# Kernel optimization log

Measured on AMD Instinct MI355X. Metric: run time of the kernel, lower is better.

The kernel has to match this reference:

```python
import jax, jax.numpy as jnp
import numpy as np

V, E, DIN, DH = 8192, 4096, 512, 256
N_CLASSES = 2
EPS = 1e-5  # torch LayerNorm default
EDGE_P = 0.004  # ~33 nodes per hyperedge


def layernorm(x, g, b):
    m = jnp.mean(x, axis=-1, keepdims=True)
    v = jnp.mean((x - m) ** 2, axis=-1, keepdims=True)
    return (x - m) / jnp.sqrt(v + EPS) * g + b


def setup_inputs() -> dict:
    key = jax.random.key(0)
    ks = jax.random.split(key, 8)
    X = jax.random.normal(ks[0], (V, DIN), dtype=jnp.float32)
    # binary incidence matrix (|V|, |E|)
    H_inc = (jax.random.uniform(ks[1], (V, E)) < EDGE_P).astype(jnp.float32)
    Wp = jax.random.normal(ks[2], (DH, DIN), dtype=jnp.float32) * 0.02  # input_proj (no bias)
    W0 = jax.random.normal(ks[3], (DH, DH), dtype=jnp.float32) * 0.02
    W1 = jax.random.normal(ks[4], (DH, DH), dtype=jnp.float32) * 0.02
    g0 = jnp.ones((DH,), jnp.float32); b0 = jnp.zeros((DH,), jnp.float32)
    g1 = jnp.ones((DH,), jnp.float32); b1 = jnp.zeros((DH,), jnp.float32)
    Wc = jax.random.normal(ks[5], (N_CLASSES, DH), dtype=jnp.float32) * 0.02
    bc = jnp.zeros((N_CLASSES,), jnp.float32)
    return {"X": X, "H_inc": H_inc, "Wp": Wp, "W0": W0, "W1": W1,
            "g0": g0, "b0": b0, "g1": g1, "b1": b1, "Wc": Wc, "bc": bc}


def reference(X, H_inc, Wp, W0, W1, g0, b0, g1, b1, Wc, bc):
    # --- normalized incidence: H_tilde = D_v^{-1/2} H D_e^{-1/2}, 0 for isolated ---
    d_v = H_inc.sum(axis=1)   # (V,)
    d_e = H_inc.sum(axis=0)   # (E,)
    dvi = jnp.where(d_v > 0, jnp.where(d_v > 0, d_v, 1.0) ** -0.5, 0.0)
    dei = jnp.where(d_e > 0, jnp.where(d_e > 0, d_e, 1.0) ** -0.5, 0.0)
    H_tilde = dvi[:, None] * H_inc * dei[None, :]            # (V, E)
    HHt = H_tilde @ H_tilde.T                                # (V, V)

    # input projection
    Xh = X @ Wp.T                                            # (V, DH)

    # L=2 message-passing layers with residual + LayerNorm
    for W, g, b in ((W0, g0, b0), (W1, g1, b1)):
        Xn = jax.nn.relu((HHt @ Xh) @ W.T)
        Xh = layernorm(Xh + Xn, g, b)

    # mean pool per hyperedge (== Python loop over E in the original):
    # z_e = mean of member node embeddings; zeros for empty hyperedges
    cnt = jnp.where(d_e > 0, d_e, 1.0)[:, None]              # (E, 1)
    z_E = (H_inc.T @ Xh) / cnt                               # (E, DH)

    logits = z_E @ Wc.T + bc                                 # (E, 2)
    return jax.nn.softmax(logits, axis=1)
```

## Files before the change

kernel.cpp:

```cpp
#include <hip/hip_runtime.h>
#include <math.h>

#define NV 8192
#define NE 4096
#define DIN 512
#define DH 256
#define CAP_E 96
#define CAP_V 64
#define NPROJ (NV / 32)
#define NSCAN (NV / 2)

#define OFF_XH   0
#define OFF_UB   (OFF_XH + NV*DH)
#define OFF_YB   (OFF_UB + NV*DH/2)
#define OFF_NCNT (OFF_YB + NE*DH/2)
#define OFF_ECNT (OFF_NCNT + NV)
#define OFF_EL   (OFF_ECNT + NE*16)
#define OFF_NL   (OFF_EL + NE*CAP_E)
#define OFF_XHB  (OFF_NL + NV*CAP_V)

using bf16x8 = __attribute__((ext_vector_type(8))) short;
using f32x4  = __attribute__((ext_vector_type(4))) float;
using f32x4v = __attribute__((ext_vector_type(4))) float;

__device__ inline unsigned short f2bf(float f) {
    union { float f; unsigned u; } v; v.f = f;
    unsigned r = v.u + 0x7FFF + ((v.u >> 16) & 1);
    return (unsigned short)(r >> 16);
}
__device__ inline float b2f(unsigned short s) {
    union { unsigned u; float f; } v; v.u = ((unsigned)s) << 16; return v.f;
}

__global__ __launch_bounds__(256) void scan_proj(const float* __restrict__ H,
                                                 const float* __restrict__ X,
                                                 const float* __restrict__ Wp,
                                                 float* __restrict__ Xh,
                                                 unsigned short* __restrict__ Xhb,
                                                 int* __restrict__ edge_cnt,
                                                 int* __restrict__ node_cnt,
                                                 int* __restrict__ edge_list,
                                                 int* __restrict__ node_list) {
    __shared__ short AsBs[1024 + 8192];
    const int tid = threadIdx.x;
    if (blockIdx.x >= NPROJ) {
        const int w = tid >> 6, lane = tid & 63;
        const int v    = (blockIdx.x - NPROJ) * 2 + (w >> 1);
        const int half = w & 1;
        const f32x4v* H4 = (const f32x4v*)(H + (size_t)v * NE) + half * 512;
        f32x4v h[8];
#pragma unroll
        for (int it = 0; it < 8; ++it)
            h[it] = __builtin_nontemporal_load(&H4[lane + 64 * it]);
        unsigned m = 0u;
#pragma unroll
        for (int it = 0; it < 8; ++it) {
#pragma unroll
            for (int c = 0; c < 4; ++c)
                m |= (h[it][c] != 0.0f ? 1u : 0u) << (it * 4 + c);
        }
        int n = __builtin_popcount(m);
        int pre = n;
#pragma unroll
        for (int o = 1; o < 64; o <<= 1) {
            int t = __shfl_up(pre, o, 64);
            if (lane >= o) pre += t;
        }
        int total = __shfl(pre, 63, 64);
        int local = pre - n;
        int base = 0;
        if (lane == 0 && total > 0) base = atomicAdd(&node_cnt[v], total);
        base = __shfl(base, 0, 64) + local;
        const int ebase = half * 2048 + 4 * lane;
        int e_arr[4] = {0, 0, 0, 0};
        {
            unsigned mm = m;
#pragma unroll
            for (int u = 0; u < 4; ++u) {
                if (mm) {
                    int j = __builtin_ctz(mm);
                    mm &= mm - 1;
                    e_arr[u] = ebase + 256 * (j >> 2) + (j & 3);
                }
            }
        }
        int s_arr[4];
#pragma unroll
        for (int u = 0; u < 4; ++u)
            s_arr[u] = (u < n) ? atomicAdd(&edge_cnt[e_arr[u] << 4], 1) : 0;
#pragma unroll
        for (int u = 0; u < 4; ++u) {
            if (u < n) {
                if (s_arr[u] < CAP_E) edge_list[e_arr[u] * CAP_E + s_arr[u]] = v;
                int idx = base + u;
                if (idx < CAP_V) node_list[v * CAP_V + idx] = e_arr[u];
            }
        }
        if (n > 4) {
            unsigned mm = m;
            mm &= mm - 1; mm &= mm - 1; mm &= mm - 1; mm &= mm - 1;
            int k = 4;
            while (mm) {
                int j = __builtin_ctz(mm); mm &= mm - 1;
                int ee = ebase + 256 * (j >> 2) + (j & 3);
                int gc = atomicAdd(&edge_cnt[ee << 4], 1);
                if (gc < CAP_E) edge_list[ee * CAP_E + gc] = v;
                int idx = base + k;
                if (idx < CAP_V) node_list[v * CAP_V + idx] = ee;
                ++k;
            }
        }
        return;
    }
    short* As = AsBs;
    short* Bs = AsBs + 1024;
    const int K = DIN;
    const int lane = tid & 63;
    const int w    = tid >> 6;
    const int bm   = blockIdx.x * 32;
    const int swz  = lane ^ ((lane >> 3) & 6);
    float4 ar, br[8];
    ar = *(const float4*)(X + (size_t)(bm + (tid >> 3)) * K + ((tid & 7) << 2));
#pragma unroll
    for (int it = 0; it < 8; ++it) {
        int i = tid + it * 256;
        br[it] = *(const float4*)(Wp + (size_t)(i >> 3) * K + ((i & 7) << 2));
    }
    f32x4 acc[2][4];
#pragma unroll
    for (int mi = 0; mi < 2; ++mi)
#pragma unroll
        for (int ni = 0; ni < 4; ++ni) acc[mi][ni] = (f32x4){0.f, 0.f, 0.f, 0.f};
    for (int k0 = 0; k0 < K; k0 += 32) {
        __syncthreads();
        {
            int row = tid >> 3, kk = (tid & 7) << 2;
            int quad = kk >> 3, j = kk & 7;
            int ln = (row & 15) + (quad << 4);
            int pp = ln ^ ((ln >> 3) & 6);
            ushort4 u = {f2bf(ar.x), f2bf(ar.y), f2bf(ar.z), f2bf(ar.w)};
            *(ushort4*)&As[(row >> 4) * 512 + pp * 8 + j] = u;
        }
#pragma unroll
        for (int it = 0; it < 8; ++it) {
            int i = tid + it * 256;
            int row = i >> 3, kk = (i & 7) << 2;
            int quad = kk >> 3, j = kk & 7;
            int ln = (row & 15) + (quad << 4);
            int pp = ln ^ ((ln >> 3) & 6);
            float4 v = br[it];
            ushort4 u = {f2bf(v.x), f2bf(v.y), f2bf(v.z), f2bf(v.w)};
            *(ushort4*)&Bs[(row >> 4) * 512 + pp * 8 + j] = u;
        }
        __syncthreads();
        if (k0 + 32 < K) {
            int kn = k0 + 32;
            ar = *(const float4*)(X + (size_t)(bm + (tid >> 3)) * K + kn + ((tid & 7) << 2));
#pragma unroll
            for (int it = 0; it < 8; ++it) {
                int i = tid + it * 256;
                br[it] = *(const float4*)(Wp + (size_t)(i >> 3) * K + kn + ((i & 7) << 2));
            }
        }
        bf16x8 af[2], bfr[4];
        af[0] = *(const bf16x8*)&As[0 * 512 + swz * 8];
        af[1] = *(const bf16x8*)&As[1 * 512 + swz * 8];
#pragma unroll
        for (int ni = 0; ni < 4; ++ni)
            bfr[ni] = *(const bf16x8*)&Bs[(w * 4 + ni) * 512 + swz * 8];
#pragma unroll
        for (int mi = 0; mi < 2; ++mi)
#pragma unroll
            for (int ni = 0; ni < 4; ++ni)
                acc[mi][ni] = __builtin_amdgcn_mfma_f32_16x16x32_bf16(
                    af[mi], bfr[ni], acc[mi][ni], 0, 0, 0);
    }
    const int quad = lane >> 4, cl = lane & 15;
#pragma unroll
    for (int mi = 0; mi < 2; ++mi)
#pragma unroll
        for (int ni = 0; ni < 4; ++ni)
#pragma unroll
            for (int r = 0; r < 4; ++r) {
                float v = acc[mi][ni][r];
                size_t idx = (size_t)(bm + mi * 16 + quad * 4 + r) * DH + w * 64 + ni * 16 + cl;
                Xh[idx] = v;
                Xhb[idx] = f2bf(v);
            }
}

__global__ __launch_bounds__(256) void gemm_u(const unsigned short* __restrict__ A,
                                              const float* __restrict__ W,
                                              unsigned short* __restrict__ U) {
    const int K = DH;
    __shared__ short As[2048];
    __shared__ short Bs[16384];
    const int tid  = threadIdx.x;
    const int lane = tid & 63;
    const int w    = tid >> 6;
    const int bm   = blockIdx.x * 32;
    const int swz  = lane ^ ((lane >> 3) & 6);

    uint4 ar; float4 br[16];
    ar = *(const uint4*)(A + (size_t)(bm + (tid >> 3)) * K + ((tid & 7) << 3));
#pragma unroll
    for (int it = 0; it < 16; ++it) {
        int i = tid + it * 256;
        br[it] = *(const float4*)(W + (size_t)(i >> 4) * K + ((i & 15) << 2));
    }
    f32x4 acc[2][4];
#pragma unroll
    for (int mi = 0; mi < 2; ++mi)
#pragma unroll
        for (int ni = 0; ni < 4; ++ni) acc[mi][ni] = (f32x4){0.f, 0.f, 0.f, 0.f};

    for (int k0 = 0; k0 < K; k0 += 64) {
        __syncthreads();
        {
            int row = tid >> 3, kq = tid & 7;
            int kc = kq >> 2, quad = kq & 3;
            int ln = (row & 15) + (quad << 4);
            int pp = ln ^ ((ln >> 3) & 6);
            *(uint4*)&As[((row >> 4) * 2 + kc) * 512 + pp * 8] = ar;
        }
#pragma unroll
        for (int it = 0; it < 16; ++it) {
            int i = tid + it * 256;
            int row = i >> 4, kk = (i & 15) << 2;
            int kc = kk >> 5, quad = (kk >> 3) & 3, j = kk & 7;
            int ln = (row & 15) + (quad << 4);
            int pp = ln ^ ((ln >> 3) & 6);
            float4 v = br[it];
            ushort4 u = {f2bf(v.x), f2bf(v.y), f2bf(v.z), f2bf(v.w)};
            *(ushort4*)&Bs[((row >> 4) * 2 + kc) * 512 + pp * 8 + j] = u;
        }
        __syncthreads();
        if (k0 + 64 < K) {
            int kn = k0 + 64;
            ar = *(const uint4*)(A + (size_t)(bm + (tid >> 3)) * K + kn + ((tid & 7) << 3));
#pragma unroll
            for (int it = 0; it < 16; ++it) {
                int i = tid + it * 256;
                br[it] = *(const float4*)(W + (size_t)(i >> 4) * K + kn + ((i & 15) << 2));
            }
        }
#pragma unroll
        for (int kc = 0; kc < 2; ++kc) {
            bf16x8 af[2], bfr[4];
            af[0] = *(const bf16x8*)&As[(0 * 2 + kc) * 512 + swz * 8];
            af[1] = *(const bf16x8*)&As[(1 * 2 + kc) * 512 + swz * 8];
#pragma unroll
            for (int ni = 0; ni < 4; ++ni)
                bfr[ni] = *(const bf16x8*)&Bs[((w * 4 + ni) * 2 + kc) * 512 + swz * 8];
#pragma unroll
            for (int mi = 0; mi < 2; ++mi)
#pragma unroll
                for (int ni = 0; ni < 4; ++ni)
                    acc[mi][ni] = __builtin_amdgcn_mfma_f32_16x16x32_bf16(
                        af[mi], bfr[ni], acc[mi][ni], 0, 0, 0);
        }
    }
    const int quad = lane >> 4, cl = lane & 15;
#pragma unroll
    for (int mi = 0; mi < 2; ++mi)
#pragma unroll
        for (int ni = 0; ni < 4; ++ni)
#pragma unroll
            for (int r = 0; r < 4; ++r)
                U[(size_t)(bm + mi * 16 + quad * 4 + r) * DH + w * 64 + ni * 16 + cl]
                    = f2bf(acc[mi][ni][r]);
}

__global__ __launch_bounds__(64) void edge_gather(const unsigned short* __restrict__ Ub,
                                                  const int* __restrict__ edge_cnt,
                                                  const int* __restrict__ edge_list,
                                                  const int* __restrict__ node_cnt,
                                                  unsigned short* __restrict__ Yb) {
    int e = blockIdx.x;
    int tid = threadIdx.x;
    __shared__ int   lv[CAP_E];
    __shared__ float lc[CAP_E];
    int tc = edge_cnt[e << 4];
    int cnt = min(tc, CAP_E);
    for (int j = tid; j < cnt; j += 64) {
        int v = edge_list[e * CAP_E + j];
        lv[j] = v * (DH / 4);
        lc[j] = rsqrtf((float)node_cnt[v]);
    }
    __syncthreads();
    const ushort4* X4 = (const ushort4*)Ub;
    float4 a[8];
#pragma unroll
    for (int u = 0; u < 8; ++u) a[u] = (float4){0.f, 0.f, 0.f, 0.f};
    int i = 0;
    for (; i + 8 <= cnt; i += 8) {
#pragma unroll
        for (int u = 0; u < 8; ++u) {
            ushort4 h = X4[lv[i + u] + tid]; float c = lc[i + u];
            a[u].x = fmaf(c, b2f(h.x), a[u].x); a[u].y = fmaf(c, b2f(h.y), a[u].y);
            a[u].z = fmaf(c, b2f(h.z), a[u].z); a[u].w = fmaf(c, b2f(h.w), a[u].w);
        }
    }
    for (; i < cnt; ++i) {
        ushort4 h = X4[lv[i] + tid]; float c = lc[i];
        a[0].x = fmaf(c, b2f(h.x), a[0].x); a[0].y = fmaf(c, b2f(h.y), a[0].y);
        a[0].z = fmaf(c, b2f(h.z), a[0].z); a[0].w = fmaf(c, b2f(h.w), a[0].w);
    }
#pragma unroll
    for (int u = 4; u > 0; u >>= 1)
#pragma unroll
        for (int q = 0; q < u; ++q) {
            a[q].x += a[q + u].x; a[q].y += a[q + u].y;
            a[q].z += a[q + u].z; a[q].w += a[q + u].w;
        }
    float de = tc > 0 ? rsqrtf((float)tc) : 0.f;
    ushort4 o = {f2bf(de * a[0].x), f2bf(de * a[0].y),
                 f2bf(de * a[0].z), f2bf(de * a[0].w)};
    ((ushort4*)Yb)[e * (DH / 4) + tid] = o;
}

__global__ __launch_bounds__(64) void node_ln(const unsigned short* __restrict__ Yb,
                                              const int* __restrict__ node_cnt,
                                              const int* __restrict__ node_list,
                                              const int* __restrict__ edge_cnt,
                                              float* __restrict__ Xh,
                                              unsigned short* __restrict__ Xhb,
                                              const float* __restrict__ g,
                                              const float* __restrict__ b) {
    int v = blockIdx.x;
    int tid = threadIdx.x;
    __shared__ int   le[CAP_V];
    __shared__ float lc[CAP_V];
    int tc = node_cnt[v];
    int cnt = min(tc, CAP_V);
    if (tid < cnt) {
        int e = node_list[v * CAP_V + tid];
        le[tid] = e * (DH / 4);
        lc[tid] = rsqrtf((float)edge_cnt[e << 4]);
    }
    __syncthreads();
    const ushort4* Y4 = (const ushort4*)Yb;
    float4 a[8];
#pragma unroll
    for (int u = 0; u < 8; ++u) a[u] = (float4){0.f, 0.f, 0.f, 0.f};
    int i = 0;
    for (; i + 8 <= cnt; i += 8) {
#pragma unroll
        for (int u = 0; u < 8; ++u) {
            ushort4 h = Y4[le[i + u] + tid]; float c = lc[i + u];
            a[u].x = fmaf(c, b2f(h.x), a[u].x); a[u].y = fmaf(c, b2f(h.y), a[u].y);
            a[u].z = fmaf(c, b2f(h.z), a[u].z); a[u].w = fmaf(c, b2f(h.w), a[u].w);
        }
    }
    for (; i < cnt; ++i) {
        ushort4 h = Y4[le[i] + tid]; float c = lc[i];
        a[0].x = fmaf(c, b2f(h.x), a[0].x); a[0].y = fmaf(c, b2f(h.y), a[0].y);
        a[0].z = fmaf(c, b2f(h.z), a[0].z); a[0].w = fmaf(c, b2f(h.w), a[0].w);
    }
#pragma unroll
    for (int u = 4; u > 0; u >>= 1)
#pragma unroll
        for (int q = 0; q < u; ++q) {
            a[q].x += a[q + u].x; a[q].y += a[q + u].y;
            a[q].z += a[q + u].z; a[q].w += a[q + u].w;
        }
    float dv = tc > 0 ? rsqrtf((float)tc) : 0.f;
    float4 xr = ((const float4*)Xh)[v * (DH / 4) + tid];
    float x0 = xr.x + fmaxf(dv * a[0].x, 0.f);
    float x1 = xr.y + fmaxf(dv * a[0].y, 0.f);
    float x2 = xr.z + fmaxf(dv * a[0].z, 0.f);
    float x3 = xr.w + fmaxf(dv * a[0].w, 0.f);
    float s = (x0 + x1) + (x2 + x3);
    float q = fmaf(x0, x0, fmaf(x1, x1, fmaf(x2, x2, x3 * x3)));
#pragma unroll
    for (int o = 1; o < 64; o <<= 1) {
        s += __shfl_xor(s, o, 64);
        q += __shfl_xor(q, o, 64);
    }
    float m = s * (1.0f / DH);
    float var = q * (1.0f / DH) - m * m;
    float rstd = rsqrtf(var + 1e-5f);
    float4 g4 = ((const float4*)g)[tid];
    float4 b4 = ((const float4*)b)[tid];
    float4 o;
    o.x = (x0 - m) * rstd * g4.x + b4.x;
    o.y = (x1 - m) * rstd * g4.y + b4.y;
    o.z = (x2 - m) * rstd * g4.z + b4.z;
    o.w = (x3 - m) * rstd * g4.w + b4.w;
    ((float4*)Xh)[v * (DH / 4) + tid] = o;
    ushort4 ob = {f2bf(o.x), f2bf(o.y), f2bf(o.z), f2bf(o.w)};
    ((ushort4*)Xhb)[v * (DH / 4) + tid] = ob;
}

__global__ __launch_bounds__(64) void pool_classify(const unsigned short* __restrict__ Xhb,
                                                    const int* __restrict__ edge_cnt,
                                                    const int* __restrict__ edge_list,
                                                    const float* __restrict__ Wc,
                                                    const float* __restrict__ bc,
                                                    float* __restrict__ out) {
    int e = blockIdx.x;
    int tid = threadIdx.x;
    __shared__ int lv[CAP_E];
    int tc = edge_cnt[e << 4];
    int cnt = min(tc, CAP_E);
    for (int j = tid; j < cnt; j += 64) lv[j] = edge_list[e * CAP_E + j] * (DH / 4);
    __syncthreads();
    const ushort4* X4 = (const ushort4*)Xhb;
    float4 a[8];
#pragma unroll
    for (int u = 0; u < 8; ++u) a[u] = (float4){0, 0, 0, 0};
    int i = 0;
    for (; i + 8 <= cnt; i += 8) {
#pragma unroll
        for (int u = 0; u < 8; ++u) {
            ushort4 h = X4[lv[i + u] + tid];
            a[u].x += b2f(h.x); a[u].y += b2f(h.y);
            a[u].z += b2f(h.z); a[u].w += b2f(h.w);
        }
    }
    for (; i < cnt; ++i) {
        ushort4 h = X4[lv[i] + tid];
        a[0].x += b2f(h.x); a[0].y += b2f(h.y);
        a[0].z += b2f(h.z); a[0].w += b2f(h.w);
    }
#pragma unroll
    for (int u = 4; u > 0; u >>= 1)
#pragma unroll
        for (int q = 0; q < u; ++q) {
            a[q].x += a[q + u].x; a[q].y += a[q + u].y;
            a[q].z += a[q + u].z; a[q].w += a[q + u].w;
        }
    float inv = tc > 0 ? 1.0f / (float)tc : 1.0f;
    float4 val = {a[0].x * inv, a[0].y * inv, a[0].z * inv, a[0].w * inv};
    const float4* W4 = (const float4*)Wc;
    float4 w0 = W4[tid], w1 = W4[64 + tid];
    float p0 = val.x * w0.x + val.y * w0.y + val.z * w0.z + val.w * w0.w;
    float p1 = val.x * w1.x + val.y * w1.y + val.z * w1.z + val.w * w1.w;
#pragma unroll
    for (int o = 32; o > 0; o >>= 1) {
        p0 += __shfl_down(p0, o, 64);
        p1 += __shfl_down(p1, o, 64);
    }
    if (tid == 0) {
        float l0 = p0 + bc[0], l1 = p1 + bc[1];
        float mx = fmaxf(l0, l1);
        float e0 = expf(l0 - mx), e1 = expf(l1 - mx);
        float s = 1.0f / (e0 + e1);
        out[e * 2 + 0] = e0 * s;
        out[e * 2 + 1] = e1 * s;
    }
}

extern "C" void kernel_launch(void* const* d_in, const int* in_sizes, int n_in,
                              void* d_out, int out_size, void* d_ws, size_t ws_size,
                              hipStream_t stream) {
    const float* X  = (const float*)d_in[0];
    const float* H  = (const float*)d_in[1];
    const float* Wp = (const float*)d_in[2];
    const float* W0 = (const float*)d_in[3];
    const float* W1 = (const float*)d_in[4];
    const float* g0 = (const float*)d_in[5];
    const float* b0 = (const float*)d_in[6];
    const float* g1 = (const float*)d_in[7];
    const float* b1 = (const float*)d_in[8];
    const float* Wc = (const float*)d_in[9];
    const float* bc = (const float*)d_in[10];
    float* out = (float*)d_out;

    float* ws = (float*)d_ws;
    float* Xh  = ws + OFF_XH;
    unsigned short* Ub  = (unsigned short*)(ws + OFF_UB);
    unsigned short* Yb  = (unsigned short*)(ws + OFF_YB);
    int* node_cnt  = (int*)(ws + OFF_NCNT);
    int* edge_cnt  = (int*)(ws + OFF_ECNT);
    int* edge_list = (int*)(ws + OFF_EL);
    int* node_list = (int*)(ws + OFF_NL);
    unsigned short* Xhb = (unsigned short*)(ws + OFF_XHB);

    hipMemsetAsync(node_cnt, 0, (size_t)(NV + NE * 16) * sizeof(int), stream);

    scan_proj<<<NPROJ + NSCAN, 256, 0, stream>>>(H, X, Wp, Xh, Xhb,
                                                 edge_cnt, node_cnt, edge_list, node_list);

    const float* Ws[2] = {W0, W1};
    const float* gs[2] = {g0, g1};
    const float* bs[2] = {b0, b1};
    for (int l = 0; l < 2; ++l) {
        gemm_u<<<NV / 32, 256, 0, stream>>>(Xhb, Ws[l], Ub);
        edge_gather<<<NE, 64, 0, stream>>>(Ub, edge_cnt, edge_list, node_cnt, Yb);
        node_ln<<<NV, 64, 0, stream>>>(Yb, node_cnt, node_list, edge_cnt,
                                       Xh, Xhb, gs[l], bs[l]);
    }

    pool_classify<<<NE, 64, 0, stream>>>(Xhb, edge_cnt, edge_list, Wc, bc, out);
}
```

Baseline: 291.2 us.

## Fuse layer GEMMs into projection and layer-0 LayerNorm epilogues via LDS

The standalone gemm_u kernel is removed. The bf16 tile of the input projection (and later of the layer-0 LayerNorm output) is written straight into swizzled LDS, and the 32x256 @ W^T GEMM is run in the same block, reading W from global and converting it to bf16 per wave. This drops two launches and the round trip of Xhb through global memory. In exchange, node_ln_u uses only 256 blocks, and each wave gathers 8 node rows one after another. That cuts parallelism for the latency-bound gather, and W is re-read per block without LDS staging.

```diff
diff --git a/kernel.cpp b/kernel.cpp
--- a/kernel.cpp
+++ b/kernel.cpp
@@ -32,11 +32,59 @@
     union { unsigned u; float f; } v; v.u = ((unsigned)s) << 16; return v.f;
 }
 
+__device__ inline void u_gemm_from_lds(const short* __restrict__ sm,
+                                       const float* __restrict__ W,
+                                       unsigned short* __restrict__ Ub,
+                                       int bm, int tid) {
+    const int w = tid >> 6, lane = tid & 63;
+    const int r15 = lane & 15, k8 = (lane >> 4) << 3;
+    const int swz = lane ^ ((lane >> 3) & 6);
+    f32x4 acc[2][4];
+#pragma unroll
+    for (int mi = 0; mi < 2; ++mi)
+#pragma unroll
+        for (int ni = 0; ni < 4; ++ni) acc[mi][ni] = (f32x4){0.f, 0.f, 0.f, 0.f};
+#pragma unroll
+    for (int kc = 0; kc < 8; ++kc) {
+        bf16x8 af[2], bfr[4];
+        af[0] = *(const bf16x8*)&sm[(0 * 8 + kc) * 512 + swz * 8];
+        af[1] = *(const bf16x8*)&sm[(1 * 8 + kc) * 512 + swz * 8];
+#pragma unroll
+        for (int ni = 0; ni < 4; ++ni) {
+            const float* wr = W + (size_t)(w * 64 + ni * 16 + r15) * DH + kc * 32 + k8;
+            float4 b0 = *(const float4*)wr;
+            float4 b1 = *(const float4*)(wr + 4);
+            bf16x8 bv;
+            bv[0] = (short)f2bf(b0.x); bv[1] = (short)f2bf(b0.y);
+            bv[2] = (short)f2bf(b0.z); bv[3] = (short)f2bf(b0.w);
+            bv[4] = (short)f2bf(b1.x); bv[5] = (short)f2bf(b1.y);
+            bv[6] = (short)f2bf(b1.z); bv[7] = (short)f2bf(b1.w);
+            bfr[ni] = bv;
+        }
+#pragma unroll
+        for (int mi = 0; mi < 2; ++mi)
+#pragma unroll
+            for (int ni = 0; ni < 4; ++ni)
+                acc[mi][ni] = __builtin_amdgcn_mfma_f32_16x16x32_bf16(
+                    af[mi], bfr[ni], acc[mi][ni], 0, 0, 0);
+    }
+    const int quad = lane >> 4, cl = lane & 15;
+#pragma unroll
+    for (int mi = 0; mi < 2; ++mi)
+#pragma unroll
+        for (int ni = 0; ni < 4; ++ni)
+#pragma unroll
+            for (int r = 0; r < 4; ++r)
+                Ub[(size_t)(bm + mi * 16 + quad * 4 + r) * DH + w * 64 + ni * 16 + cl]
+                    = f2bf(acc[mi][ni][r]);
+}
+
 __global__ __launch_bounds__(256) void scan_proj(const float* __restrict__ H,
                                                  const float* __restrict__ X,
                                                  const float* __restrict__ Wp,
+                                                 const float* __restrict__ W0,
                                                  float* __restrict__ Xh,
-                                                 unsigned short* __restrict__ Xhb,
+                                                 unsigned short* __restrict__ Ub,
                                                  int* __restrict__ edge_cnt,
                                                  int* __restrict__ node_cnt,
                                                  int* __restrict__ edge_list,
@@ -176,6 +224,7 @@
                     af[mi], bfr[ni], acc[mi][ni], 0, 0, 0);
     }
     const int quad = lane >> 4, cl = lane & 15;
+    __syncthreads();
 #pragma unroll
     for (int mi = 0; mi < 2; ++mi)
 #pragma unroll
@@ -183,92 +232,17 @@
 #pragma unroll
             for (int r = 0; r < 4; ++r) {
                 float v = acc[mi][ni][r];
-                size_t idx = (size_t)(bm + mi * 16 + quad * 4 + r) * DH + w * 64 + ni * 16 + cl;
-                Xh[idx] = v;
-                Xhb[idx] = f2bf(v);
-            }
-}
-
-__global__ __launch_bounds__(256) void gemm_u(const unsigned short* __restrict__ A,
-                                              const float* __restrict__ W,
-                                              unsigned short* __restrict__ U) {
-    const int K = DH;
-    __shared__ short As[2048];
-    __shared__ short Bs[16384];
-    const int tid  = threadIdx.x;
-    const int lane = tid & 63;
-    const int w    = tid >> 6;
-    const int bm   = blockIdx.x * 32;
-    const int swz  = lane ^ ((lane >> 3) & 6);
-
-    uint4 ar; float4 br[16];
-    ar = *(const uint4*)(A + (size_t)(bm + (tid >> 3)) * K + ((tid & 7) << 3));
-#pragma unroll
-    for (int it = 0; it < 16; ++it) {
-        int i = tid + it * 256;
-        br[it] = *(const float4*)(W + (size_t)(i >> 4) * K + ((i & 15) << 2));
-    }
-    f32x4 acc[2][4];
-#pragma unroll
-    for (int mi = 0; mi < 2; ++mi)
-#pragma unroll
-        for (int ni = 0; ni < 4; ++ni) acc[mi][ni] = (f32x4){0.f, 0.f, 0.f, 0.f};
-
-    for (int k0 = 0; k0 < K; k0 += 64) {
-        __syncthreads();
-        {
-            int row = tid >> 3, kq = tid & 7;
-            int kc = kq >> 2, quad = kq & 3;
-            int ln = (row & 15) + (quad << 4);
-            int pp = ln ^ ((ln >> 3) & 6);
-            *(uint4*)&As[((row >> 4) * 2 + kc) * 512 + pp * 8] = ar;
-        }
-#pragma unroll
-        for (int it = 0; it < 16; ++it) {
-            int i = tid + it * 256;
-            int row = i >> 4, kk = (i & 15) << 2;
-            int kc = kk >> 5, quad = (kk >> 3) & 3, j = kk & 7;
-            int ln = (row & 15) + (quad << 4);
-            int pp = ln ^ ((ln >> 3) & 6);
-            float4 v = br[it];
-            ushort4 u = {f2bf(v.x), f2bf(v.y), f2bf(v.z), f2bf(v.w)};
-            *(ushort4*)&Bs[((row >> 4) * 2 + kc) * 512 + pp * 8 + j] = u;
-        }
-        __syncthreads();
-        if (k0 + 64 < K) {
-            int kn = k0 + 64;
-            ar = *(const uint4*)(A + (size_t)(bm + (tid >> 3)) * K + kn + ((tid & 7) << 3));
-#pragma unroll
-            for (int it = 0; it < 16; ++it) {
-                int i = tid + it * 256;
-                br[it] = *(const float4*)(W + (size_t)(i >> 4) * K + kn + ((i & 15) << 2));
-            }
-        }
-#pragma unroll
-        for (int kc = 0; kc < 2; ++kc) {
-            bf16x8 af[2], bfr[4];
-            af[0] = *(const bf16x8*)&As[(0 * 2 + kc) * 512 + swz * 8];
-            af[1] = *(const bf16x8*)&As[(1 * 2 + kc) * 512 + swz * 8];
-#pragma unroll
-            for (int ni = 0; ni < 4; ++ni)
-                bfr[ni] = *(const bf16x8*)&Bs[((w * 4 + ni) * 2 + kc) * 512 + swz * 8];
-#pragma unroll
-            for (int mi = 0; mi < 2; ++mi)
-#pragma unroll
-                for (int ni = 0; ni < 4; ++ni)
-                    acc[mi][ni] = __builtin_amdgcn_mfma_f32_16x16x32_bf16(
-                        af[mi], bfr[ni], acc[mi][ni], 0, 0, 0);
-        }
-    }
-    const int quad = lane >> 4, cl = lane & 15;
-#pragma unroll
-    for (int mi = 0; mi < 2; ++mi)
-#pragma unroll
-        for (int ni = 0; ni < 4; ++ni)
-#pragma unroll
-            for (int r = 0; r < 4; ++r)
-                U[(size_t)(bm + mi * 16 + quad * 4 + r) * DH + w * 64 + ni * 16 + cl]
-                    = f2bf(acc[mi][ni][r]);
+                int rl  = mi * 16 + quad * 4 + r;
+                int col = w * 64 + ni * 16 + cl;
+                Xh[(size_t)(bm + rl) * DH + col] = v;
+                int kc = col >> 5, kk = col & 31;
+                int q2 = kk >> 3, j = kk & 7;
+                int ln = (rl & 15) + (q2 << 4);
+                int pp = ln ^ ((ln >> 3) & 6);
+                AsBs[(mi * 8 + kc) * 512 + pp * 8 + j] = (short)f2bf(v);
+            }
+    __syncthreads();
+    u_gemm_from_lds(AsBs, W0, Ub, bm, tid);
 }
 
 __global__ __launch_bounds__(64) void edge_gather(const unsigned short* __restrict__ Ub,
@@ -317,6 +291,93 @@
     ushort4 o = {f2bf(de * a[0].x), f2bf(de * a[0].y),
                  f2bf(de * a[0].z), f2bf(de * a[0].w)};
     ((ushort4*)Yb)[e * (DH / 4) + tid] = o;
+}
+
+__global__ __launch_bounds__(256) void node_ln_u(const unsigned short* __restrict__ Yb,
+                                                 const int* __restrict__ node_cnt,
+                                                 const int* __restrict__ node_list,
+                                                 const int* __restrict__ edge_cnt,
+                                                 float* __restrict__ Xh,
+                                                 const float* __restrict__ g,
+                                                 const float* __restrict__ b,
+                                                 const float* __restrict__ W1,
+                                                 unsigned short* __restrict__ Ub) {
+    __shared__ short sm[9216];
+    const int tid = threadIdx.x;
+    const int w = tid >> 6, lane = tid & 63;
+    const int bm = blockIdx.x * 32;
+    int* lbase = (int*)&sm[8192];
+    int*   lep = lbase + w * 128;
+    float* lcp = (float*)(lbase + w * 128 + 64);
+    for (int ii = 0; ii < 8; ++ii) {
+        const int rl = ii * 4 + w;
+        const int v  = bm + rl;
+        int tc = node_cnt[v];
+        int cnt = min(tc, CAP_V);
+        if (lane < cnt) {
+            int e = node_list[v * CAP_V + lane];
+            lep[lane] = e * (DH / 4);
+            lcp[lane] = rsqrtf((float)edge_cnt[e << 4]);
+        }
+        __syncthreads();
+        const ushort4* Y4 = (const ushort4*)Yb;
+        float4 a[8];
+#pragma unroll
+        for (int u = 0; u < 8; ++u) a[u] = (float4){0.f, 0.f, 0.f, 0.f};
+        int i = 0;
+        for (; i + 8 <= cnt; i += 8) {
+#pragma unroll
+            for (int u = 0; u < 8; ++u) {
+                ushort4 h = Y4[lep[i + u] + lane]; float c = lcp[i + u];
+                a[u].x = fmaf(c, b2f(h.x), a[u].x); a[u].y = fmaf(c, b2f(h.y), a[u].y);
+                a[u].z = fmaf(c, b2f(h.z), a[u].z); a[u].w = fmaf(c, b2f(h.w), a[u].w);
+            }
+        }
+        for (; i < cnt; ++i) {
+            ushort4 h = Y4[lep[i] + lane]; float c = lcp[i];
+            a[0].x = fmaf(c, b2f(h.x), a[0].x); a[0].y = fmaf(c, b2f(h.y), a[0].y);
+            a[0].z = fmaf(c, b2f(h.z), a[0].z); a[0].w = fmaf(c, b2f(h.w), a[0].w);
+        }
+#pragma unroll
+        for (int u = 4; u > 0; u >>= 1)
+#pragma unroll
+            for (int q = 0; q < u; ++q) {
+                a[q].x += a[q + u].x; a[q].y += a[q + u].y;
+                a[q].z += a[q + u].z; a[q].w += a[q + u].w;
+            }
+        float dv = tc > 0 ? rsqrtf((float)tc) : 0.f;
+        float4 xr = ((const float4*)Xh)[v * (DH / 4) + lane];
+        float x0 = xr.x + fmaxf(dv * a[0].x, 0.f);
+        float x1 = xr.y + fmaxf(dv * a[0].y, 0.f);
+        float x2 = xr.z + fmaxf(dv * a[0].z, 0.f);
+        float x3 = xr.w + fmaxf(dv * a[0].w, 0.f);
+        float s = (x0 + x1) + (x2 + x3);
+        float q = fmaf(x0, x0, fmaf(x1, x1, fmaf(x2, x2, x3 * x3)));
+#pragma unroll
+        for (int o = 1; o < 64; o <<= 1) {
+            s += __shfl_xor(s, o, 64);
+            q += __shfl_xor(q, o, 64);
+        }
+        float m = s * (1.0f / DH);
+        float var = q * (1.0f / DH) - m * m;
+        float rstd = rsqrtf(var + 1e-5f);
+        float4 g4 = ((const float4*)g)[lane];
+        float4 b4 = ((const float4*)b)[lane];
+        float4 o;
+        o.x = (x0 - m) * rstd * g4.x + b4.x;
+        o.y = (x1 - m) * rstd * g4.y + b4.y;
+        o.z = (x2 - m) * rstd * g4.z + b4.z;
+        o.w = (x3 - m) * rstd * g4.w + b4.w;
+        ((float4*)Xh)[v * (DH / 4) + lane] = o;
+        ushort4 ob = {f2bf(o.x), f2bf(o.y), f2bf(o.z), f2bf(o.w)};
+        int mi = rl >> 4, kc = lane >> 3;
+        int q2 = (lane & 7) >> 1, jj = (lane & 1) * 4;
+        int ln = (rl & 15) + (q2 << 4);
+        int pp = ln ^ ((ln >> 3) & 6);
+        *(ushort4*)&sm[(mi * 8 + kc) * 512 + pp * 8 + jj] = ob;
+        __syncthreads();
+    }
+    u_gemm_from_lds(sm, W1, Ub, bm, tid);
 }
 
 __global__ __launch_bounds__(64) void node_ln(const unsigned short* __restrict__ Yb,
@@ -479,18 +540,15 @@
 
     hipMemsetAsync(node_cnt, 0, (size_t)(NV + NE * 16) * sizeof(int), stream);
 
-    scan_proj<<<NPROJ + NSCAN, 256, 0, stream>>>(H, X, Wp, Xh, Xhb,
+    scan_proj<<<NPROJ + NSCAN, 256, 0, stream>>>(H, X, Wp, W0, Xh, Ub,
                                                  edge_cnt, node_cnt, edge_list, node_list);
 
-    const float* Ws[2] = {W0, W1};
-    const float* gs[2] = {g0, g1};
-    const float* bs[2] = {b0, b1};
-    for (int l = 0; l < 2; ++l) {
-        gemm_u<<<NV / 32, 256, 0, stream>>>(Xhb, Ws[l], Ub);
-        edge_gather<<<NE, 64, 0, stream>>>(Ub, edge_cnt, edge_list, node_cnt, Yb);
-        node_ln<<<NV, 64, 0, stream>>>(Yb, node_cnt, node_list, edge_cnt,
-                                       Xh, Xhb, gs[l], bs[l]);
-    }
+    edge_gather<<<NE, 64, 0, stream>>>(Ub, edge_cnt, edge_list, node_cnt, Yb);
+    node_ln_u<<<NV / 32, 256, 0, stream>>>(Yb, node_cnt, node_list, edge_cnt,
+                                           Xh, g0, b0, W1, Ub);
+    edge_gather<<<NE, 64, 0, stream>>>(Ub, edge_cnt, edge_list, node_cnt, Yb);
+    node_ln<<<NV, 64, 0, stream>>>(Yb, node_cnt, node_list, edge_cnt,
+                                   Xh, Xhb, g1, b1);
 
     pool_classify<<<NE, 64, 0, stream>>>(Xhb, edge_cnt, edge_list, Wc, bc, out);
 }
```

After: 305.2 us. +4.8%, slower.
